# Optimization experiments

Measured on AMD Instinct MI355X. Metric: run time of the kernel, lower is better.

## Reference

```python
import jax, jax.numpy as jnp
import numpy as np

B, S, E, H = 8, 8192, 512, 64
DK = E // H  # 8 quantum wires per head

# Math note: the circuit is RX(x_i) then RX(phi_i) on each wire i of |0..0>,
# followed by <PauliZ_i>. All gates act on disjoint wires, so the state stays a
# product state and RX(a)RX(b) = RX(a+b). For RX(t)|0>, <Z> = cos(t).
# Hence the exact circuit output is cos(x + phi) elementwise (same math,
# without materializing the 2^DK state vector).

def setup_inputs() -> dict:
    key = jax.random.key(0)
    k1, k2, k3, k4 = jax.random.split(key, 4)
    x = jax.random.normal(k1, (B, S, E), dtype=jnp.float32)
    # trainable RX angles, one per wire, shared across heads (single QLayer instance)
    phi = jax.random.uniform(k2, (DK,), dtype=jnp.float32, minval=-np.pi, maxval=np.pi)
    bound = 1.0 / np.sqrt(E)
    W_combine = jax.random.uniform(k3, (E, E), dtype=jnp.float32, minval=-bound, maxval=bound)
    b_combine = jax.random.uniform(k4, (E,), dtype=jnp.float32, minval=-bound, maxval=bound)
    return {"x": x, "phi": phi, "W_combine": W_combine, "b_combine": b_combine}

def reference(x, phi, W_combine, b_combine):
    b, s, e = x.shape
    xh = x.reshape(b, s, H, DK)            # [B,S,H,DK] per-head wire angles
    qz = jnp.cos(xh + phi)                 # <Z_i> of RX(x)+RX(phi) circuit
    out = qz.reshape(b, s, e)              # concat heads back to embed_dim
    return out @ W_combine.T + b_combine   # combine Linear
```

## Files before the change

### kernel.cpp

```cpp
#include <hip/hip_runtime.h>
#include <hip/hip_bf16.h>

typedef __bf16 bf16_t;
typedef bf16_t bf16x4 __attribute__((ext_vector_type(4)));
typedef bf16_t bf16x8 __attribute__((ext_vector_type(8)));
typedef float  f32x4  __attribute__((ext_vector_type(4)));

constexpr int M_TOT = 65536;
constexpr int N_TOT = 512;
constexpr int K_TOT = 512;
constexpr int BM = 128, BN = 128, BK = 64;

__device__ inline void gload_lds16(const void* g, void* l) {
    __builtin_amdgcn_global_load_lds(
        (const __attribute__((address_space(1))) void*)g,
        (__attribute__((address_space(3))) void*)l, 16, 0, 0);
}

__global__ __launch_bounds__(256)
void convert_W(const float* __restrict__ W, bf16_t* __restrict__ Wws)
{
    const int g  = blockIdx.x * 256 + threadIdx.x;
    const int n  = g >> 6;
    const int c  = g & 63;
    const int kt = c >> 3, ck = c & 7;
    const float4* src = reinterpret_cast<const float4*>(W + (size_t)n * K_TOT + c * 8);
    float4 v0 = src[0], v1 = src[1];
    bf16x8 b;
    b[0] = (bf16_t)v0.x; b[1] = (bf16_t)v0.y; b[2] = (bf16_t)v0.z; b[3] = (bf16_t)v0.w;
    b[4] = (bf16_t)v1.x; b[5] = (bf16_t)v1.y; b[6] = (bf16_t)v1.z; b[7] = (bf16_t)v1.w;
    const int dc = kt * 64 + ((ck ^ (n & 7)) * 8);
    *reinterpret_cast<bf16x8*>(Wws + (size_t)n * K_TOT + dc) = b;
}

template<bool USE_WS>
__global__ __launch_bounds__(256, 3)
void qattn_fused_gemm(const float* __restrict__ x,
                      const float* __restrict__ phi,
                      const float* __restrict__ W,
                      const bf16_t* __restrict__ Wws,
                      const float* __restrict__ bias,
                      float* __restrict__ out)
{
    __shared__ bf16_t As[BM][BK];
    __shared__ bf16_t Bs[BN][BK];

    const int tid  = threadIdx.x;
    const int lane = tid & 63;
    const int wave = tid >> 6;

    const int xcd = blockIdx.x & 7;
    const int idx = blockIdx.x >> 3;
    const int wid = xcd * 256 + idx;
    const int bm  = (wid >> 2) * BM;
    const int bn  = (wid & 3)  * BN;

    const int srow = tid >> 4;
    const int scol = (tid & 15) * 4;

    const int pbase = scol & 4;
    const float p0 = phi[pbase + 0];
    const float p1 = phi[pbase + 1];
    const float p2 = phi[pbase + 2];
    const float p3 = phi[pbase + 3];

    const int wm   = (wave >> 1) * 64;
    const int wn   = (wave & 1) * 64;
    const int frow = lane & 15;
    const int fk   = (lane >> 4) * 8;

    f32x4 acc[4][4] = {};

    float4 pa[8];
    #pragma unroll
    for (int p = 0; p < 8; ++p) {
        const int row = srow + p * 16;
        pa[p] = *reinterpret_cast<const float4*>(x + (size_t)(bm + row) * K_TOT + scol);
    }

    for (int k0 = 0; k0 < K_TOT; k0 += BK) {
        if (USE_WS) {
            #pragma unroll
            for (int i = 0; i < 4; ++i) {
                const int chunk = lane & 7;
                const int row   = wave * 32 + i * 8 + (lane >> 3);
                const bf16_t* src = Wws + (size_t)(bn + row) * K_TOT + k0 + chunk * 8;
                gload_lds16(src, &Bs[0][0] + wave * 2048 + i * 512);
            }
        } else {
            #pragma unroll
            for (int p = 0; p < 8; ++p) {
                const int row = srow + p * 16;
                const int csw = scol ^ ((row & 7) << 3);
                float4 w = *reinterpret_cast<const float4*>(
                    W + (size_t)(bn + row) * K_TOT + k0 + scol);
                bf16x4 b;
                b[0] = (bf16_t)w.x; b[1] = (bf16_t)w.y;
                b[2] = (bf16_t)w.z; b[3] = (bf16_t)w.w;
                *reinterpret_cast<bf16x4*>(&Bs[row][csw]) = b;
            }
        }

        #pragma unroll
        for (int p = 0; p < 8; ++p) {
            const int row = srow + p * 16;
            const int csw = scol ^ ((row & 7) << 3);
            bf16x4 a;
            a[0] = (bf16_t)__cosf(pa[p].x + p0);
            a[1] = (bf16_t)__cosf(pa[p].y + p1);
            a[2] = (bf16_t)__cosf(pa[p].z + p2);
            a[3] = (bf16_t)__cosf(pa[p].w + p3);
            *reinterpret_cast<bf16x4*>(&As[row][csw]) = a;
        }

        {
            const int knext = (k0 + BK < K_TOT) ? k0 + BK : 0;
            #pragma unroll
            for (int p = 0; p < 8; ++p) {
                const int row = srow + p * 16;
                pa[p] = *reinterpret_cast<const float4*>(
                    x + (size_t)(bm + row) * K_TOT + knext + scol);
            }
        }

        if (USE_WS)
            asm volatile("s_waitcnt vmcnt(8) lgkmcnt(0)\n\ts_barrier" ::: "memory");
        else
            __syncthreads();

        #pragma unroll
        for (int kk = 0; kk < 2; ++kk) {
            bf16x8 af[4], bfr[4];
            #pragma unroll
            for (int mi = 0; mi < 4; ++mi) {
                const int r = wm + mi * 16 + frow;
                const int c = (kk * 32 + fk) ^ ((r & 7) << 3);
                af[mi] = *reinterpret_cast<bf16x8*>(&As[r][c]);
            }
            #pragma unroll
            for (int ni = 0; ni < 4; ++ni) {
                const int r = wn + ni * 16 + frow;
                const int c = (kk * 32 + fk) ^ ((r & 7) << 3);
                bfr[ni] = *reinterpret_cast<bf16x8*>(&Bs[r][c]);
            }
            #pragma unroll
            for (int mi = 0; mi < 4; ++mi)
                #pragma unroll
                for (int ni = 0; ni < 4; ++ni)
                    acc[mi][ni] = __builtin_amdgcn_mfma_f32_16x16x32_bf16(
                        af[mi], bfr[ni], acc[mi][ni], 0, 0, 0);
        }

        if (USE_WS)
            asm volatile("s_waitcnt lgkmcnt(0)\n\ts_barrier" ::: "memory");
        else
            __syncthreads();
    }

    #pragma unroll
    for (int ni = 0; ni < 4; ++ni) {
        const int c  = bn + wn + ni * 16 + (lane & 15);
        const float bv = bias[c];
        #pragma unroll
        for (int mi = 0; mi < 4; ++mi) {
            const int r0 = bm + wm + mi * 16 + (lane >> 4) * 4;
            #pragma unroll
            for (int i = 0; i < 4; ++i)
                out[(size_t)(r0 + i) * N_TOT + c] = acc[mi][ni][i] + bv;
        }
    }
}

extern "C" void kernel_launch(void* const* d_in, const int* in_sizes, int n_in,
                              void* d_out, int out_size, void* d_ws, size_t ws_size,
                              hipStream_t stream) {
    const float* x    = (const float*)d_in[0];
    const float* phi  = (const float*)d_in[1];
    const float* W    = (const float*)d_in[2];
    const float* bias = (const float*)d_in[3];
    float* out = (float*)d_out;

    const int grid = (M_TOT / BM) * (N_TOT / BN);
    const size_t ws_need = (size_t)N_TOT * K_TOT * sizeof(bf16_t);

    if (ws_size >= ws_need) {
        bf16_t* Wws = (bf16_t*)d_ws;
        convert_W<<<(N_TOT * K_TOT / 8) / 256, 256, 0, stream>>>(W, Wws);
        qattn_fused_gemm<true><<<grid, 256, 0, stream>>>(x, phi, W, Wws, bias, out);
    } else {
        qattn_fused_gemm<false><<<grid, 256, 0, stream>>>(x, phi, W, nullptr, bias, out);
    }
}
```

Measured before the change: 75.31 us.

## Feed A fragments directly from registers and double-buffer B tile in LDS

```diff
diff --git a/kernel.cpp b/kernel.cpp
--- a/kernel.cpp
+++ b/kernel.cpp
@@ -2,7 +2,6 @@
 #include <hip/hip_bf16.h>
 
 typedef __bf16 bf16_t;
-typedef bf16_t bf16x4 __attribute__((ext_vector_type(4)));
 typedef bf16_t bf16x8 __attribute__((ext_vector_type(8)));
 typedef float  f32x4  __attribute__((ext_vector_type(4)));
 
@@ -10,6 +9,7 @@
 constexpr int N_TOT = 512;
 constexpr int K_TOT = 512;
 constexpr int BM = 128, BN = 128, BK = 64;
+constexpr int NT = K_TOT / BK;
 
 __device__ inline void gload_lds16(const void* g, void* l) {
     __builtin_amdgcn_global_load_lds(
@@ -42,8 +42,7 @@
                       const float* __restrict__ bias,
                       float* __restrict__ out)
 {
-    __shared__ bf16_t As[BM][BK];
-    __shared__ bf16_t Bs[BN][BK];
+    __shared__ bf16_t Bs[2][BN][BK];
 
     const int tid  = threadIdx.x;
     const int lane = tid & 63;
@@ -55,115 +54,136 @@
     const int bm  = (wid >> 2) * BM;
     const int bn  = (wid & 3)  * BN;
 
-    const int srow = tid >> 4;
-    const int scol = (tid & 15) * 4;
-
-    const int pbase = scol & 4;
-    const float p0 = phi[pbase + 0];
-    const float p1 = phi[pbase + 1];
-    const float p2 = phi[pbase + 2];
-    const float p3 = phi[pbase + 3];
-
-    const int wm   = (wave >> 1) * 64;
-    const int wn   = (wave & 1) * 64;
+    float ph[8];
+    #pragma unroll
+    for (int j = 0; j < 8; ++j) ph[j] = phi[j];
+
     const int frow = lane & 15;
     const int fk   = (lane >> 4) * 8;
 
-    f32x4 acc[4][4] = {};
-
+    const float* xb = x + (size_t)(bm + wave * 32 + frow) * K_TOT + fk;
+
+    f32x4  acc[2][8] = {};
     float4 pa[8];
-    #pragma unroll
-    for (int p = 0; p < 8; ++p) {
-        const int row = srow + p * 16;
-        pa[p] = *reinterpret_cast<const float4*>(x + (size_t)(bm + row) * K_TOT + scol);
-    }
-
-    for (int k0 = 0; k0 < K_TOT; k0 += BK) {
-        if (USE_WS) {
+
+    if constexpr (USE_WS) {
+        #pragma unroll
+        for (int i = 0; i < 4; ++i) {
+            const bf16_t* src = Wws + (size_t)(bn + wave * 32 + i * 8 + (lane >> 3)) * K_TOT
+                                + (lane & 7) * 8;
+            gload_lds16(src, &Bs[0][0][0] + wave * 2048 + i * 512);
+        }
+        __builtin_amdgcn_sched_barrier(0);
+    } else {
+        const int brow = tid >> 1;
+        #pragma unroll
+        for (int i = 0; i < 4; ++i) {
+            const int ck = (tid & 1) * 4 + i;
+            const float4* s = reinterpret_cast<const float4*>(
+                W + (size_t)(bn + brow) * K_TOT + ck * 8);
+            float4 v0 = s[0], v1 = s[1];
+            bf16x8 b;
+            b[0] = (bf16_t)v0.x; b[1] = (bf16_t)v0.y; b[2] = (bf16_t)v0.z; b[3] = (bf16_t)v0.w;
+            b[4] = (bf16_t)v1.x; b[5] = (bf16_t)v1.y; b[6] = (bf16_t)v1.z; b[7] = (bf16_t)v1.w;
+            *reinterpret_cast<bf16x8*>(&Bs[0][brow][(ck ^ (brow & 7)) * 8]) = b;
+        }
+    }
+    #pragma unroll
+    for (int f = 0; f < 8; ++f) {
+        const int mi = f >> 2, kk = (f >> 1) & 1, h = f & 1;
+        pa[f] = *reinterpret_cast<const float4*>(xb + mi * 16 * K_TOT + kk * 32 + h * 4);
+    }
+    if constexpr (USE_WS)
+        asm volatile("s_waitcnt vmcnt(8) lgkmcnt(0)\n\ts_barrier" ::: "memory");
+    else
+        asm volatile("s_waitcnt lgkmcnt(0)\n\ts_barrier" ::: "memory");
+
+    #pragma unroll
+    for (int t = 0; t < NT; ++t) {
+        const int cur  = t & 1;
+        const bool last = (t == NT - 1);
+        const int kn   = (t + 1) * BK;
+
+        if (!last) {
+            if constexpr (USE_WS) {
+                #pragma unroll
+                for (int i = 0; i < 4; ++i) {
+                    const bf16_t* src = Wws
+                        + (size_t)(bn + wave * 32 + i * 8 + (lane >> 3)) * K_TOT
+                        + kn + (lane & 7) * 8;
+                    gload_lds16(src, &Bs[cur ^ 1][0][0] + wave * 2048 + i * 512);
+                }
+                __builtin_amdgcn_sched_barrier(0);
+            } else {
+                const int brow = tid >> 1;
+                #pragma unroll
+                for (int i = 0; i < 4; ++i) {
+                    const int ck = (tid & 1) * 4 + i;
+                    const float4* s = reinterpret_cast<const float4*>(
+                        W + (size_t)(bn + brow) * K_TOT + kn + ck * 8);
+                    float4 v0 = s[0], v1 = s[1];
+                    bf16x8 b;
+                    b[0] = (bf16_t)v0.x; b[1] = (bf16_t)v0.y; b[2] = (bf16_t)v0.z; b[3] = (bf16_t)v0.w;
+                    b[4] = (bf16_t)v1.x; b[5] = (bf16_t)v1.y; b[6] = (bf16_t)v1.z; b[7] = (bf16_t)v1.w;
+                    *reinterpret_cast<bf16x8*>(&Bs[cur ^ 1][brow][(ck ^ (brow & 7)) * 8]) = b;
+                }
+            }
+        }
+
+        bf16x8 af[2][2];
+        #pragma unroll
+        for (int f = 0; f < 8; ++f) {
+            const int mi = f >> 2, kk = (f >> 1) & 1, h = f & 1;
+            af[mi][kk][h * 4 + 0] = (bf16_t)__cosf(pa[f].x + ph[h * 4 + 0]);
+            af[mi][kk][h * 4 + 1] = (bf16_t)__cosf(pa[f].y + ph[h * 4 + 1]);
+            af[mi][kk][h * 4 + 2] = (bf16_t)__cosf(pa[f].z + ph[h * 4 + 2]);
+            af[mi][kk][h * 4 + 3] = (bf16_t)__cosf(pa[f].w + ph[h * 4 + 3]);
+        }
+
+        if (!last) {
             #pragma unroll
-            for (int i = 0; i < 4; ++i) {
-                const int chunk = lane & 7;
-                const int row   = wave * 32 + i * 8 + (lane >> 3);
-                const bf16_t* src = Wws + (size_t)(bn + row) * K_TOT + k0 + chunk * 8;
-                gload_lds16(src, &Bs[0][0] + wave * 2048 + i * 512);
+            for (int f = 0; f < 8; ++f) {
+                const int mi = f >> 2, kk = (f >> 1) & 1, h = f & 1;
+                pa[f] = *reinterpret_cast<const float4*>(
+                    xb + mi * 16 * K_TOT + kn + kk * 32 + h * 4);
             }
-        } else {
+        }
+
+        #pragma unroll
+        for (int kk = 0; kk < 2; ++kk) {
             #pragma unroll
-            for (int p = 0; p < 8; ++p) {
-                const int row = srow + p * 16;
-                const int csw = scol ^ ((row & 7) << 3);
-                float4 w = *reinterpret_cast<const float4*>(
-                    W + (size_t)(bn + row) * K_TOT + k0 + scol);
-                bf16x4 b;
-                b[0] = (bf16_t)w.x; b[1] = (bf16_t)w.y;
-                b[2] = (bf16_t)w.z; b[3] = (bf16_t)w.w;
-                *reinterpret_cast<bf16x4*>(&Bs[row][csw]) = b;
+            for (int nh = 0; nh < 2; ++nh) {
+                bf16x8 bfr[4];
+                #pragma unroll
+                for (int nj = 0; nj < 4; ++nj) {
+                    const int r = (nh * 4 + nj) * 16 + frow;
+                    const int c = (kk * 32 + fk) ^ ((r & 7) << 3);
+                    bfr[nj] = *reinterpret_cast<const bf16x8*>(&Bs[cur][r][c]);
+                }
+                #pragma unroll
+                for (int mi = 0; mi < 2; ++mi)
+                    #pragma unroll
+                    for (int nj = 0; nj < 4; ++nj)
+                        acc[mi][nh * 4 + nj] = __builtin_amdgcn_mfma_f32_16x16x32_bf16(
+                            af[mi][kk], bfr[nj], acc[mi][nh * 4 + nj], 0, 0, 0);
             }
         }
 
-        #pragma unroll
-        for (int p = 0; p < 8; ++p) {
-            const int row = srow + p * 16;
-            const int csw = scol ^ ((row & 7) << 3);
-            bf16x4 a;
-            a[0] = (bf16_t)__cosf(pa[p].x + p0);
-            a[1] = (bf16_t)__cosf(pa[p].y + p1);
-            a[2] = (bf16_t)__cosf(pa[p].z + p2);
-            a[3] = (bf16_t)__cosf(pa[p].w + p3);
-            *reinterpret_cast<bf16x4*>(&As[row][csw]) = a;
-        }
-
-        {
-            const int knext = (k0 + BK < K_TOT) ? k0 + BK : 0;
-            #pragma unroll
-            for (int p = 0; p < 8; ++p) {
-                const int row = srow + p * 16;
-                pa[p] = *reinterpret_cast<const float4*>(
-                    x + (size_t)(bm + row) * K_TOT + knext + scol);
-            }
-        }
-
-        if (USE_WS)
-            asm volatile("s_waitcnt vmcnt(8) lgkmcnt(0)\n\ts_barrier" ::: "memory");
-        else
-            __syncthreads();
-
-        #pragma unroll
-        for (int kk = 0; kk < 2; ++kk) {
-            bf16x8 af[4], bfr[4];
-            #pragma unroll
-            for (int mi = 0; mi < 4; ++mi) {
-                const int r = wm + mi * 16 + frow;
-                const int c = (kk * 32 + fk) ^ ((r & 7) << 3);
-                af[mi] = *reinterpret_cast<bf16x8*>(&As[r][c]);
-            }
-            #pragma unroll
-            for (int ni = 0; ni < 4; ++ni) {
-                const int r = wn + ni * 16 + frow;
-                const int c = (kk * 32 + fk) ^ ((r & 7) << 3);
-                bfr[ni] = *reinterpret_cast<bf16x8*>(&Bs[r][c]);
-            }
-            #pragma unroll
-            for (int mi = 0; mi < 4; ++mi)
-                #pragma unroll
-                for (int ni = 0; ni < 4; ++ni)
-                    acc[mi][ni] = __builtin_amdgcn_mfma_f32_16x16x32_bf16(
-                        af[mi], bfr[ni], acc[mi][ni], 0, 0, 0);
-        }
-
-        if (USE_WS)
-            asm volatile("s_waitcnt lgkmcnt(0)\n\ts_barrier" ::: "memory");
-        else
-            __syncthreads();
-    }
-
-    #pragma unroll
-    for (int ni = 0; ni < 4; ++ni) {
-        const int c  = bn + wn + ni * 16 + (lane & 15);
+        if (!last) {
+            if constexpr (USE_WS)
+                asm volatile("s_waitcnt vmcnt(8) lgkmcnt(0)\n\ts_barrier" ::: "memory");
+            else
+                asm volatile("s_waitcnt lgkmcnt(0)\n\ts_barrier" ::: "memory");
+        }
+    }
+
+    #pragma unroll
+    for (int ni = 0; ni < 8; ++ni) {
+        const int c  = bn + ni * 16 + frow;
         const float bv = bias[c];
         #pragma unroll
-        for (int mi = 0; mi < 4; ++mi) {
-            const int r0 = bm + wm + mi * 16 + (lane >> 4) * 4;
+        for (int mi = 0; mi < 2; ++mi) {
+            const int r0 = bm + wave * 32 + mi * 16 + (lane >> 4) * 4;
             #pragma unroll
             for (int i = 0; i < 4; ++i)
                 out[(size_t)(r0 + i) * N_TOT + c] = acc[mi][ni][i] + bv;
```

New measurement: 95.63 us. 1.27x slower.
